# Kernel optimization log

Hardware: AMD Instinct MI355X
Metric: run time of the kernel (lower is better)

The kernel has to match this reference:

```python
import jax, jax.numpy as jnp
import numpy as np

HS, WS = 64, 64
SIGMA = 1.2
UPDATE_COEFF = 0.2
R = 3
N_BLOCKS = 3
GROUPS = 8
EPS_GN = 1e-5
CM, CP, CS, CT, HID = 64, 3, 128, 128, 128
B, T, HIN, WIN = 32, 256, 128, 128


def setup_inputs() -> dict:
    key = jax.random.key(0)
    ks = jax.random.split(key, 10)
    s = 0.02
    cin = CM + CP + CT
    f32 = jnp.float32
    return {
        'M': jax.random.normal(ks[0], (B, CM, HIN, WIN), f32),
        'x0_hat_norm': jax.random.uniform(ks[1], (B, T, 2), f32, -1.0, 1.0),
        't_embed': jax.random.normal(ks[2], (B, CT), f32),
        'in_proj_w': jax.random.normal(ks[3], (CS, cin), f32) * s,
        'in_proj_b': jnp.zeros((CS,), f32),
        'rb_c1w': jax.random.normal(ks[4], (N_BLOCKS, CS, CS, 3, 3), f32) * s,
        'rb_c1b': jnp.zeros((N_BLOCKS, CS), f32),
        'rb_g1w': jnp.ones((N_BLOCKS, CS), f32),
        'rb_g1b': jnp.zeros((N_BLOCKS, CS), f32),
        'rb_c2w': jax.random.normal(ks[5], (N_BLOCKS, CS, CS, 3, 3), f32) * s,
        'rb_c2b': jnp.zeros((N_BLOCKS, CS), f32),
        'rb_g2w': jnp.ones((N_BLOCKS, CS), f32),
        'rb_g2b': jnp.zeros((N_BLOCKS, CS), f32),
        'out_w': jax.random.normal(ks[6], (CS, CS), f32) * s,
        'out_b': jnp.zeros((CS,), f32),
        'mlp_w1': jax.random.normal(ks[7], (CS + CT, HID), f32) * s,
        'mlp_b1': jnp.zeros((HID,), f32),
        'mlp_w2': jax.random.normal(ks[8], (HID, HID), f32) * s,
        'mlp_b2': jnp.zeros((HID,), f32),
        'mlp_w3': jax.random.normal(ks[9], (HID, 2), f32) * s,
        'mlp_b3': jnp.zeros((2,), f32),
    }


def _resize_bilinear(M, Hs, Ws):
    # torch F.interpolate bilinear, align_corners=False, no antialias
    Bn, C, H, W = M.shape
    def coords(n_out, n_in):
        sc = n_in / n_out
        c = (jnp.arange(n_out, dtype=M.dtype) + 0.5) * sc - 0.5
        c = jnp.clip(c, 0.0, n_in - 1.0)
        i0 = jnp.floor(c)
        f = c - i0
        i0 = i0.astype(jnp.int32)
        i1 = jnp.minimum(i0 + 1, n_in - 1)
        return i0, i1, f
    y0, y1, fy = coords(Hs, H)
    x0, x1, fx = coords(Ws, W)
    top = M[:, :, y0, :] * (1 - fy)[None, None, :, None] + M[:, :, y1, :] * fy[None, None, :, None]
    return top[:, :, :, x0] * (1 - fx)[None, None, None, :] + top[:, :, :, x1] * fx[None, None, None, :]


def _rasterize_vel(pts, H, W, sigma):
    # pts: (B,T,2) pixel coords -> (B,3,H,W) [heat, vx, vy]
    xs = jnp.arange(W, dtype=pts.dtype)
    ys = jnp.arange(H, dtype=pts.dtype)
    d2 = (pts[:, :, None, None, 0] - xs[None, None, None, :]) ** 2 \
       + (pts[:, :, None, None, 1] - ys[None, None, :, None]) ** 2  # (B,T,H,W)
    w = jnp.exp(-0.5 * d2 / (sigma ** 2 + 1e-8))
    heat = w.max(axis=1)
    v = jnp.pad(jnp.diff(pts, axis=1), ((0, 0), (1, 0), (0, 0)))
    vx = (w * v[:, :, None, None, 0]).sum(axis=1)
    vy = (w * v[:, :, None, None, 1]).sum(axis=1)
    wsum = jnp.maximum(w.sum(axis=1), 1e-6)
    return jnp.stack([heat, vx / wsum, vy / wsum], axis=1)


def _conv3x3(x, w, b):
    y = jax.lax.conv_general_dilated(x, w, (1, 1), 'SAME', dimension_numbers=('NCHW', 'OIHW', 'NCHW'))
    return y + b[None, :, None, None]


def _gn(x, g, b):
    Bn, C, H, W = x.shape
    xr = x.reshape(Bn, GROUPS, C // GROUPS, H, W)
    mu = xr.mean(axis=(2, 3, 4), keepdims=True)
    var = xr.var(axis=(2, 3, 4), keepdims=True)
    xn = ((xr - mu) * jax.lax.rsqrt(var + EPS_GN)).reshape(Bn, C, H, W)
    return xn * g[None, :, None, None] + b[None, :, None, None]


def _grid_sample(S, coords):
    # bilinear, align_corners=False, zero padding. coords (B,T,2) in [-1,1] -> (B,T,C)
    Bn, C, H, W = S.shape
    Tn = coords.shape[1]
    x = ((coords[..., 0] + 1.0) * W - 1.0) * 0.5
    y = ((coords[..., 1] + 1.0) * H - 1.0) * 0.5
    x0 = jnp.floor(x)
    y0 = jnp.floor(y)
    wx = x - x0
    wy = y - y0
    Sf = S.reshape(Bn, C, H * W)
    out = jnp.zeros((Bn, C, Tn), S.dtype)
    for xi, yi, wgt in ((x0, y0, (1 - wx) * (1 - wy)), (x0 + 1, y0, wx * (1 - wy)),
                        (x0, y0 + 1, (1 - wx) * wy), (x0 + 1, y0 + 1, wx * wy)):
        valid = (xi >= 0) & (xi <= W - 1) & (yi >= 0) & (yi <= H - 1)
        xc = jnp.clip(xi, 0, W - 1).astype(jnp.int32)
        yc = jnp.clip(yi, 0, H - 1).astype(jnp.int32)
        idx = jnp.broadcast_to((yc * W + xc)[:, None, :], (Bn, C, Tn))
        g = jnp.take_along_axis(Sf, idx, axis=2)
        out = out + g * (wgt * valid)[:, None, :]
    return out.transpose(0, 2, 1)


def _forward(M, x0_hat_norm, t_embed, in_proj_w, in_proj_b, rb_c1w, rb_c1b, rb_g1w, rb_g1b,
             rb_c2w, rb_c2b, rb_g2w, rb_g2b, out_w, out_b,
             mlp_w1, mlp_b1, mlp_w2, mlp_b2, mlp_w3, mlp_b3):
    Bn = M.shape[0]
    Ms = _resize_bilinear(M, HS, WS)
    t_map = jnp.broadcast_to(t_embed[:, :, None, None], (Bn, CT, HS, WS))
    x = x0_hat_norm
    for _ in range(R):
        x_pix = jnp.stack([(x[..., 0] + 1) * 0.5 * (WS - 1), (x[..., 1] + 1) * 0.5 * (HS - 1)], axis=-1)
        P = _rasterize_vel(x_pix, HS, WS, SIGMA)  # (B,3,HS,WS)
        # SpatialRefine
        inp = jnp.concatenate([Ms, P, t_map], axis=1)
        S = jnp.einsum('bihw,oi->bohw', inp, in_proj_w) + in_proj_b[None, :, None, None]
        for i in range(N_BLOCKS):
            h = jax.nn.silu(_gn(_conv3x3(S, rb_c1w[i], rb_c1b[i]), rb_g1w[i], rb_g1b[i]))
            h = _gn(_conv3x3(h, rb_c2w[i], rb_c2b[i]), rb_g2w[i], rb_g2b[i])
            S = jax.nn.silu(S + h)
        S = jnp.einsum('bihw,oi->bohw', S, out_w) + out_b[None, :, None, None]
        # PointCorrector
        read = _grid_sample(S, x)  # (B,T,CS)
        t_tok = jnp.broadcast_to(t_embed[:, None, :], (Bn, read.shape[1], CT))
        feat = jnp.concatenate([read, t_tok], axis=-1)
        h = jax.nn.silu(feat @ mlp_w1 + mlp_b1)
        h = jax.nn.silu(h @ mlp_w2 + mlp_b2)
        dx = h @ mlp_w3 + mlp_b3
        x = jnp.clip(x + UPDATE_COEFF * dx, -1.0, 1.0)
    return x


def reference(M, x0_hat_norm, t_embed, in_proj_w, in_proj_b, rb_c1w, rb_c1b, rb_g1w, rb_g1b,
              rb_c2w, rb_c2b, rb_g2w, rb_g2b, out_w, out_b,
              mlp_w1, mlp_b1, mlp_w2, mlp_b2, mlp_w3, mlp_b3):
    return _forward(M, x0_hat_norm, t_embed, in_proj_w, in_proj_b, rb_c1w, rb_c1b, rb_g1w, rb_g1b,
                    rb_c2w, rb_c2b, rb_g2w, rb_g2b, out_w, out_b,
                    mlp_w1, mlp_b1, mlp_w2, mlp_b2, mlp_w3, mlp_b3)
```

## Files before the change

### kernel.cpp

```cpp
#include <hip/hip_runtime.h>
#include <cstddef>

#define BN 32
#define TN 256
#define PW 66
#define PLANE 4356

typedef __attribute__((ext_vector_type(8))) short bf16x8;
typedef __attribute__((ext_vector_type(4))) float f32x4;

struct __attribute__((aligned(16))) U4 { unsigned x, y, z, w; };

__device__ __forceinline__ float silu_f(float v) { return v / (1.f + __expf(-v)); }

__device__ __forceinline__ unsigned short f2bf(float f) {
  unsigned u = __float_as_uint(f);
  unsigned r = (u + 0x7fffu + ((u >> 16) & 1u)) >> 16;
  return (unsigned short)r;
}
__device__ __forceinline__ float bf2f(unsigned short h) {
  return __uint_as_float((unsigned)h << 16);
}
__device__ __forceinline__ unsigned pack2(float a, float b) {
  return (unsigned)f2bf(a) | ((unsigned)f2bf(b) << 16);
}

__device__ __forceinline__ void gld16(const unsigned short* g, unsigned short* l) {
  __builtin_amdgcn_global_load_lds((const __attribute__((address_space(1))) unsigned int*)g,
                                   (__attribute__((address_space(3))) unsigned int*)l, 16, 0, 0);
}

__global__ __launch_bounds__(256) void copy_kernel(const float* __restrict__ src, float* __restrict__ dst, int n) {
  int i = blockIdx.x * 256 + threadIdx.x;
  if (i < n) dst[i] = src[i];
}

__global__ __launch_bounds__(256) void zerohalo_kernel(unsigned short* __restrict__ base) {
  int idx = blockIdx.x * 256 + threadIdx.x;
  if (idx >= 384 * 1040) return;
  int p = idx / 1040, rem = idx % 1040;
  int hp = rem >> 2, icq = rem & 3;
  int row, x;
  if (hp < 66) { row = 0; x = hp; }
  else if (hp < 132) { row = 65; x = hp - 66; }
  else { int i = hp - 132; row = 1 + (i >> 1); x = (i & 1) * 65; }
  U4 z = {0u, 0u, 0u, 0u};
  *(U4*)&base[((size_t)p * PLANE + row * PW + x) * 32 + icq * 8] = z;
}

__global__ __launch_bounds__(256) void resize_t_kernel(const float* __restrict__ M, unsigned short* __restrict__ Ms4) {
  __shared__ unsigned short lt[4 * 64 * 72];
  int b = blockIdx.y, yt = blockIdx.x;
  int tid = threadIdx.x;
  for (int i = tid; i < 4 * 64 * 64; i += 256) {
    int c = i >> 8, y = (i >> 6) & 3, x = i & 63;
    const float* p = M + (((size_t)(b * 64 + c) * 128) + (yt * 4 + y) * 2) * 128 + 2 * x;
    float2 a = *(const float2*)p;
    float2 bq = *(const float2*)(p + 128);
    lt[(y * 64 + x) * 72 + c] = f2bf(0.25f * (a.x + a.y + bq.x + bq.y));
  }
  __syncthreads();
  for (int i = tid; i < 2048; i += 256) {
    int icq = i & 3, pxl = (i >> 2) & 255, cc = i >> 10;
    U4 q = *(const U4*)&lt[pxl * 72 + cc * 32 + icq * 8];
    int y = yt * 4 + (pxl >> 6), x = pxl & 63;
    *(U4*)&Ms4[(((size_t)(b * 2 + cc) * PLANE) + (size_t)(y + 1) * PW + x + 1) * 32 + icq * 8] = q;
  }
}

__global__ __launch_bounds__(256) void wprep_kernel(const float* __restrict__ Wsrc, unsigned short* __restrict__ Wdst) {
  int idx = blockIdx.x * 256 + threadIdx.x;
  if (idx >= 147456) return;
  int icp = idx & 31;
  int oc = (idx >> 5) & 127;
  int tc = idx >> 12;
  int t = tc >> 2, cch = tc & 3;
  Wdst[idx] = f2bf(Wsrc[(size_t)oc * 1152 + (size_t)(cch * 32 + icp) * 9 + t]);
}

__global__ __launch_bounds__(256) void wprep_in_kernel(const float* __restrict__ ipw, unsigned short* __restrict__ wi) {
  int idx = blockIdx.x * 256 + threadIdx.x;
  if (idx >= 12288) return;
  int icp = idx & 31, oc = (idx >> 5) & 127, cc = idx >> 12;
  float f = 0.f;
  if (cc < 2) f = ipw[oc * 195 + cc * 32 + icp];
  else if (icp < 3) f = ipw[oc * 195 + 64 + icp];
  wi[idx] = f2bf(f);
}

__global__ __launch_bounds__(256) void wprep_out_kernel(const float* __restrict__ ow, unsigned short* __restrict__ wo) {
  int idx = blockIdx.x * 256 + threadIdx.x;
  if (idx >= 16384) return;
  int icp = idx & 31, oc = (idx >> 5) & 127, cc = idx >> 12;
  wo[idx] = f2bf(ow[oc * 128 + cc * 32 + icp]);
}

__global__ __launch_bounds__(256) void tctr_kernel(const float* __restrict__ w, const float* __restrict__ bias,
                                                   const float* __restrict__ te, float* __restrict__ tctr) {
  int i = blockIdx.x * 256 + threadIdx.x;
  if (i >= BN * 128) return;
  int b = i >> 7, o = i & 127;
  float acc = bias[o];
  const float* wp = w + (size_t)o * 195 + 67;
  const float* t = te + b * 128;
  #pragma unroll 8
  for (int k = 0; k < 128; ++k) acc += wp[k] * t[k];
  tctr[i] = acc;
}

__global__ __launch_bounds__(256) void tpart_kernel(const float* __restrict__ w1, const float* __restrict__ b1,
                                                    const float* __restrict__ te, float* __restrict__ tp) {
  int i = blockIdx.x * 256 + threadIdx.x;
  if (i >= BN * 128) return;
  int b = i >> 7, j = i & 127;
  float acc = b1[j];
  #pragma unroll 8
  for (int k = 0; k < 128; ++k) acc += te[b * 128 + k] * w1[(size_t)(128 + k) * 128 + j];
  tp[i] = acc;
}

__global__ __launch_bounds__(256) void raster4_kernel(const float* __restrict__ x, unsigned short* __restrict__ Pp) {
  int b = blockIdx.y, blk = blockIdx.x;
  int tid = threadIdx.x;
  int pix = blk * 256 + tid;
  __shared__ float spx[TN], spy[TN];
  __shared__ unsigned short lp[256 * 32];
  spx[tid] = (x[(b * TN + tid) * 2] + 1.f) * 0.5f * 63.f;
  spy[tid] = (x[(b * TN + tid) * 2 + 1] + 1.f) * 0.5f * 63.f;
  __syncthreads();
  float fx = (float)(pix & 63), fy = (float)(pix >> 6);
  const float coef = -0.5f / (1.44f + 1e-8f);
  float heat = 0.f, sx = 0.f, sy = 0.f, sw = 0.f;
  float prevx = 0.f, prevy = 0.f;
  for (int t = 0; t < TN; ++t) {
    float px = spx[t], py = spy[t];
    float ddx = px - fx, ddy = py - fy;
    float w = __expf(coef * (ddx * ddx + ddy * ddy));
    heat = fmaxf(heat, w);
    float vx = (t == 0) ? 0.f : px - prevx;
    float vy = (t == 0) ? 0.f : py - prevy;
    prevx = px; prevy = py;
    sx += w * vx; sy += w * vy; sw += w;
  }
  float inv = 1.f / fmaxf(sw, 1e-6f);
  U4 q0; q0.x = pack2(heat, sx * inv); q0.y = pack2(sy * inv, 0.f); q0.z = 0u; q0.w = 0u;
  U4 z = {0u, 0u, 0u, 0u};
  *(U4*)&lp[tid * 32 + 0] = q0;
  *(U4*)&lp[tid * 32 + 8] = z;
  *(U4*)&lp[tid * 32 + 16] = z;
  *(U4*)&lp[tid * 32 + 24] = z;
  __syncthreads();
  for (int it = 0; it < 4; ++it) {
    int sid = it * 256 + tid;
    int pxl = sid >> 2, icq = sid & 3;
    int gp = blk * 256 + pxl;
    int y = gp >> 6, xx = gp & 63;
    *(U4*)&Pp[((size_t)b * PLANE + (size_t)(y + 1) * PW + xx + 1) * 32 + icq * 8] = *(const U4*)&lp[pxl * 32 + icq * 8];
  }
}

__global__ __launch_bounds__(512, 4) void conv3_v4(const unsigned short* __restrict__ In4,
                                                   const unsigned short* __restrict__ Wb,
                                                   const float* __restrict__ Bias,
                                                   unsigned short* __restrict__ Out4) {
  __shared__ unsigned short lds[2][12672];
  const int P = blockIdx.x;
  const int L = (P & 7) * 64 + (P >> 3);
  const int b = L >> 4, y0 = (L & 15) * 4;
  const int tid = threadIdx.x, l = tid & 63, w = tid >> 6;
  const int ocg = w & 1, rowg = w >> 1, l15 = l & 15, k8 = l >> 4;

  f32x4 acc[4][4];
  #pragma unroll
  for (int mf = 0; mf < 4; ++mf)
    #pragma unroll
    for (int nf = 0; nf < 4; ++nf) acc[mf][nf] = (f32x4){0.f, 0.f, 0.f, 0.f};

  auto issue_stage = [&](int cc, int nb) {
    const unsigned short* slab = In4 + (((size_t)(b * 4 + cc)) * PLANE + (size_t)y0 * PW) * 32;
    #pragma unroll
    for (int i = 0; i < 3; ++i) {
      int G = i * 512 + tid;
      int q = G >> 2;
      int r = q / 66;
      int xs = q - r * 66;
      int src = (G & ~3) | ((G & 3) ^ ((xs >> 1) & 3));
      gld16(slab + (size_t)src * 8, &lds[nb][(size_t)(i * 512 + w * 64) * 8]);
    }
    if (tid < 96) {
      int G = 1536 + tid;
      int q = G >> 2;
      int r = q / 66;
      int xs = q - r * 66;
      int src = (G & ~3) | ((G & 3) ^ ((xs >> 1) & 3));
      gld16(slab + (size_t)src * 8, &lds[nb][(size_t)(1536 + w * 64) * 8]);
    }
  };

  issue_stage(0, 0);
  __syncthreads();

  for (int cc = 0; cc < 4; ++cc) {
    const unsigned short* cur = &lds[cc & 1][0];
    if (cc < 3) issue_stage(cc + 1, (cc & 1) ^ 1);
    #pragma unroll
    for (int t = 0; t < 9; ++t) {
      const int ky = t / 3, kx = t - ky * 3;
      bf16x8 a[4];
      #pragma unroll
      for (int mf = 0; mf < 4; ++mf)
        a[mf] = *(const bf16x8*)&Wb[(((size_t)(t * 4 + cc) * 128) + ocg * 64 + mf * 16 + l15) * 32 + k8 * 8];
      #pragma unroll
      for (int nf = 0; nf < 4; ++nf) {
        int xs = nf * 16 + l15 + kx;
        int slot = ((rowg + ky) * 66 + xs) * 4 + (k8 ^ ((xs >> 1) & 3));
        bf16x8 bv = *(const bf16x8*)&cur[(size_t)slot * 8];
        #pragma unroll
        for (int mf = 0; mf < 4; ++mf)
          acc[mf][nf] = __builtin_amdgcn_mfma_f32_16x16x32_bf16(a[mf], bv, acc[mf][nf], 0, 0, 0);
      }
    }
    __syncthreads();
  }

  unsigned short* eb = &lds[0][0];
  #pragma unroll
  for (int h = 0; h < 2; ++h) {
    if ((rowg >> 1) == h) {
      int prow = rowg & 1;
      #pragma unroll
      for (int mf = 0; mf < 4; ++mf) {
        int oc = ocg * 64 + mf * 16 + k8 * 4;
        float4 bv4 = *(const float4*)&Bias[oc];
        #pragma unroll
        for (int nf = 0; nf < 4; ++nf) {
          int pxl = prow * 64 + nf * 16 + l15;
          unsigned lo = pack2(acc[mf][nf][0] + bv4.x, acc[mf][nf][1] + bv4.y);
          unsigned hi = pack2(acc[mf][nf][2] + bv4.z, acc[mf][nf][3] + bv4.w);
          unsigned off = (unsigned)(pxl * 256 + oc * 2) ^ ((pxl & 7) << 4);
          *(uint2*)((char*)eb + off) = make_uint2(lo, hi);
        }
      }
    }
    __syncthreads();
    {
      int pxl = tid >> 2, icq = tid & 3;
      int px = h * 128 + pxl;
      int yy = px >> 6, xx = px & 63;
      #pragma unroll
      for (int cc2 = 0; cc2 < 4; ++cc2) {
        unsigned off = (unsigned)(pxl * 256 + cc2 * 64 + icq * 16) ^ ((pxl & 7) << 4);
        U4 q = *(const U4*)((char*)eb + off);
        *(U4*)&Out4[(((size_t)(b * 4 + cc2)) * PLANE + (size_t)(y0 + yy + 1) * PW + xx + 1) * 32 + icq * 8] = q;
      }
    }
    __syncthreads();
  }
}

__global__ __launch_bounds__(256, 2) void conv1_v2(const unsigned short* __restrict__ srcA, int ncA,
                                                   const unsigned short* __restrict__ srcB, int nc,
                                                   const unsigned short* __restrict__ Wb,
                                                   const float* __restrict__ Bias, int perB,
                                                   unsigned short* __restrict__ Out4) {
  __shared__ unsigned short lds[32768];
  const int P = blockIdx.x;
  const int L = (P & 7) * 64 + (P >> 3);
  const int b = L >> 4, px0 = (L & 15) * 256;
  const int tid = threadIdx.x, l = tid & 63, w = tid >> 6;
  const int ocg = w & 1, rowg = w >> 1, l15 = l & 15, k8 = l >> 4;

  f32x4 acc[4][8];
  #pragma unroll
  for (int mf = 0; mf < 4; ++mf)
    #pragma unroll
    for (int nf = 0; nf < 8; ++nf) acc[mf][nf] = (f32x4){0.f, 0.f, 0.f, 0.f};

  for (int cc = 0; cc < nc; ++cc) {
    const unsigned short* base = (cc < ncA) ? srcA + ((size_t)(b * ncA + cc)) * PLANE * 32
                                            : srcB + ((size_t)b) * PLANE * 32;
    bf16x8 a[4];
    #pragma unroll
    for (int mf = 0; mf < 4; ++mf)
      a[mf] = *(const bf16x8*)&Wb[(((size_t)cc * 128) + ocg * 64 + mf * 16 + l15) * 32 + k8 * 8];
    #pragma unroll
    for (int nf = 0; nf < 8; ++nf) {
      int px = px0 + rowg * 128 + nf * 16 + l15;
      int y = px >> 6, x = px & 63;
      bf16x8 bv = *(const bf16x8*)&base[((size_t)(y + 1) * PW + x + 1) * 32 + k8 * 8];
      #pragma unroll
      for (int mf = 0; mf < 4; ++mf)
        acc[mf][nf] = __builtin_amdgcn_mfma_f32_16x16x32_bf16(a[mf], bv, acc[mf][nf], 0, 0, 0);
    }
  }
  const float* bp = Bias + (perB ? b * 128 : 0);
  #pragma unroll
  for (int mf = 0; mf < 4; ++mf) {
    int oc = ocg * 64 + mf * 16 + k8 * 4;
    float4 bv4 = *(const float4*)&bp[oc];
    #pragma unroll
    for (int nf = 0; nf < 8; ++nf) {
      int pxl = rowg * 128 + nf * 16 + l15;
      unsigned lo = pack2(acc[mf][nf][0] + bv4.x, acc[mf][nf][1] + bv4.y);
      unsigned hi = pack2(acc[mf][nf][2] + bv4.z, acc[mf][nf][3] + bv4.w);
      unsigned off = (unsigned)(pxl * 256 + oc * 2) ^ ((pxl & 7) << 4);
      *(uint2*)((char*)lds + off) = make_uint2(lo, hi);
    }
  }
  __syncthreads();
  #pragma unroll
  for (int cc2 = 0; cc2 < 4; ++cc2)
    #pragma unroll
    for (int it = 0; it < 4; ++it) {
      int sid = it * 256 + tid;
      int pxl = sid >> 2, icq = sid & 3;
      unsigned off = (unsigned)(pxl * 256 + cc2 * 64 + icq * 16) ^ ((pxl & 7) << 4);
      U4 q = *(const U4*)((char*)lds + off);
      int px = px0 + pxl;
      int yy = px >> 6, xx = px & 63;
      *(U4*)&Out4[(((size_t)(b * 4 + cc2)) * PLANE + (size_t)(yy + 1) * PW + xx + 1) * 32 + icq * 8] = q;
    }
}

__global__ __launch_bounds__(256) void gnstats4_kernel(const unsigned short* __restrict__ X, float* __restrict__ stats) {
  int bc = blockIdx.x;
  const unsigned short* p = X + (size_t)bc * PLANE * 32;
  float s0 = 0.f, q0 = 0.f, s1 = 0.f, q1 = 0.f;
  for (int px = threadIdx.x; px < 4096; px += 256) {
    const unsigned short* row = p + ((size_t)((px >> 6) + 1) * PW + (px & 63) + 1) * 32;
    #pragma unroll
    for (int half = 0; half < 2; ++half) {
      float s = 0.f, qq = 0.f;
      #pragma unroll
      for (int ii = 0; ii < 2; ++ii) {
        U4 v = *(const U4*)&row[half * 16 + ii * 8];
        unsigned a[4] = {v.x, v.y, v.z, v.w};
        #pragma unroll
        for (int p2 = 0; p2 < 4; ++p2) {
          float f0 = bf2f((unsigned short)(a[p2] & 0xffffu));
          float f1 = bf2f((unsigned short)(a[p2] >> 16));
          s += f0 + f1; qq += f0 * f0 + f1 * f1;
        }
      }
      if (half == 0) { s0 += s; q0 += qq; } else { s1 += s; q1 += qq; }
    }
  }
  __shared__ float red[4][256];
  red[0][threadIdx.x] = s0; red[1][threadIdx.x] = q0; red[2][threadIdx.x] = s1; red[3][threadIdx.x] = q1;
  __syncthreads();
  for (int off = 128; off > 0; off >>= 1) {
    if (threadIdx.x < off)
      #pragma unroll
      for (int k = 0; k < 4; ++k) red[k][threadIdx.x] += red[k][threadIdx.x + off];
    __syncthreads();
  }
  if (threadIdx.x == 0) {
    const float invn = 1.f / 65536.f;
    int b = bc >> 2, cc = bc & 3;
    float mu0 = red[0][0] * invn, var0 = red[1][0] * invn - mu0 * mu0;
    float mu1 = red[2][0] * invn, var1 = red[3][0] * invn - mu1 * mu1;
    int g0 = b * 8 + cc * 2;
    stats[g0 * 2] = mu0; stats[g0 * 2 + 1] = rsqrtf(var0 + 1e-5f);
    stats[(g0 + 1) * 2] = mu1; stats[(g0 + 1) * 2 + 1] = rsqrtf(var1 + 1e-5f);
  }
}

__global__ __launch_bounds__(256) void gn1apply_kernel(unsigned short* __restrict__ A,
                                                       const float* __restrict__ stats, const float* __restrict__ gam,
                                                       const float* __restrict__ bet) {
  size_t e8 = (size_t)blockIdx.x * 256 + threadIdx.x;
  int icq = (int)(e8 & 3), x = (int)((e8 >> 2) & 63), y = (int)((e8 >> 8) & 63);
  int cc = (int)((e8 >> 14) & 3), b = (int)(e8 >> 16);
  size_t off = (((size_t)(b * 4 + cc)) * PLANE + (size_t)(y + 1) * PW + x + 1) * 32 + icq * 8;
  int ch = icq * 8;
  int g = cc * 2 + (ch >> 4);
  float mu = stats[(b * 8 + g) * 2], ri = stats[(b * 8 + g) * 2 + 1];
  int c0 = cc * 32 + ch;
  float4 g0 = *(const float4*)&gam[c0], g1 = *(const float4*)&gam[c0 + 4];
  float4 b0 = *(const float4*)&bet[c0], b1 = *(const float4*)&bet[c0 + 4];
  float gv[8] = {g0.x, g0.y, g0.z, g0.w, g1.x, g1.y, g1.z, g1.w};
  float bv[8] = {b0.x, b0.y, b0.z, b0.w, b1.x, b1.y, b1.z, b1.w};
  U4 va = *(const U4*)&A[off];
  unsigned aa[4] = {va.x, va.y, va.z, va.w};
  unsigned out[4];
  #pragma unroll
  for (int p = 0; p < 4; ++p) {
    float h0 = (bf2f((unsigned short)(aa[p] & 0xffffu)) - mu) * ri * gv[2 * p] + bv[2 * p];
    float h1 = (bf2f((unsigned short)(aa[p] >> 16)) - mu) * ri * gv[2 * p + 1] + bv[2 * p + 1];
    out[p] = pack2(silu_f(h0), silu_f(h1));
  }
  U4 q; q.x = out[0]; q.y = out[1]; q.z = out[2]; q.w = out[3];
  *(U4*)&A[off] = q;
}

__global__ __launch_bounds__(256) void gn2add4_kernel(unsigned short* __restrict__ S, const unsigned short* __restrict__ Bb,
                                                      const float* __restrict__ stats, const float* __restrict__ gam,
                                                      const float* __restrict__ bet) {
  size_t e8 = (size_t)blockIdx.x * 256 + threadIdx.x;
  int icq = (int)(e8 & 3), x = (int)((e8 >> 2) & 63), y = (int)((e8 >> 8) & 63);
  int cc = (int)((e8 >> 14) & 3), b = (int)(e8 >> 16);
  size_t off = (((size_t)(b * 4 + cc)) * PLANE + (size_t)(y + 1) * PW + x + 1) * 32 + icq * 8;
  int ch = icq * 8;
  int g = cc * 2 + (ch >> 4);
  float mu = stats[(b * 8 + g) * 2], ri = stats[(b * 8 + g) * 2 + 1];
  int c0 = cc * 32 + ch;
  float4 g0 = *(const float4*)&gam[c0], g1 = *(const float4*)&gam[c0 + 4];
  float4 b0 = *(const float4*)&bet[c0], b1 = *(const float4*)&bet[c0 + 4];
  float gv[8] = {g0.x, g0.y, g0.z, g0.w, g1.x, g1.y, g1.z, g1.w};
  float bv[8] = {b0.x, b0.y, b0.z, b0.w, b1.x, b1.y, b1.z, b1.w};
  U4 vb = *(const U4*)&Bb[off];
  U4 vs = *(const U4*)&S[off];
  unsigned ab[4] = {vb.x, vb.y, vb.z, vb.w};
  unsigned as[4] = {vs.x, vs.y, vs.z, vs.w};
  unsigned out[4];
  #pragma unroll
  for (int p = 0; p < 4; ++p) {
    float h0 = (bf2f((unsigned short)(ab[p] & 0xffffu)) - mu) * ri * gv[2 * p] + bv[2 * p];
    float h1 = (bf2f((unsigned short)(ab[p] >> 16)) - mu) * ri * gv[2 * p + 1] + bv[2 * p + 1];
    float r0 = silu_f(bf2f((unsigned short)(as[p] & 0xffffu)) + h0);
    float r1 = silu_f(bf2f((unsigned short)(as[p] >> 16)) + h1);
    out[p] = pack2(r0, r1);
  }
  U4 q; q.x = out[0]; q.y = out[1]; q.z = out[2]; q.w = out[3];
  *(U4*)&S[off] = q;
}

__global__ __launch_bounds__(128) void gsample4_kernel(const unsigned short* __restrict__ S2, const float* __restrict__ x,
                                                       float* __restrict__ rd) {
  int token = blockIdx.x, c = threadIdx.x, b = token >> 8;
  float cx = x[token * 2], cy = x[token * 2 + 1];
  float fx = (cx + 1.f) * 32.f - 0.5f;
  float fy = (cy + 1.f) * 32.f - 0.5f;
  float x0f = floorf(fx), y0f = floorf(fy);
  float wx = fx - x0f, wy = fy - y0f;
  const unsigned short* Sb = S2 + ((size_t)(b * 4 + (c >> 5)) * PLANE) * 32 + (c & 31);
  float acc = 0.f;
  #pragma unroll
  for (int cor = 0; cor < 4; ++cor) {
    float xi = x0f + (float)(cor & 1), yi = y0f + (float)(cor >> 1);
    float wgt = ((cor & 1) ? wx : 1.f - wx) * ((cor >> 1) ? wy : 1.f - wy);
    if (xi >= 0.f && xi <= 63.f && yi >= 0.f && yi <= 63.f)
      acc += bf2f(Sb[(size_t)(((int)yi + 1) * PW + (int)xi + 1) * 32]) * wgt;
  }
  rd[(size_t)token * 128 + c] = acc;
}

__global__ __launch_bounds__(256) void mlp_fc_kernel(const float* __restrict__ in, const float* __restrict__ w,
                                                     const float* __restrict__ init, int initPerB,
                                                     float* __restrict__ out) {
  int tok0 = blockIdx.x * 2;
  int tid = threadIdx.x;
  __shared__ float sr[2][128];
  sr[tid >> 7][tid & 127] = in[(size_t)tok0 * 128 + tid];
  __syncthreads();
  int t = tid >> 7, j = tid & 127;
  int token = tok0 + t;
  int b = token >> 8;
  float acc = initPerB ? init[b * 128 + j] : init[j];
  #pragma unroll 8
  for (int k = 0; k < 128; ++k) acc += sr[t][k] * w[(size_t)k * 128 + j];
  out[(size_t)token * 128 + j] = silu_f(acc);
}

__global__ __launch_bounds__(256) void mlp3_update_kernel(const float* __restrict__ h2, const float* __restrict__ w3,
                                                          const float* __restrict__ b3, float* __restrict__ x) {
  int token = blockIdx.x * 256 + threadIdx.x;
  if (token >= BN * TN) return;
  float d0 = b3[0], d1 = b3[1];
  const float* h = h2 + (size_t)token * 128;
  #pragma unroll 8
  for (int k = 0; k < 128; ++k) { float hv = h[k]; d0 += hv * w3[k * 2]; d1 += hv * w3[k * 2 + 1]; }
  float nx = x[token * 2] + 0.2f * d0;
  float ny = x[token * 2 + 1] + 0.2f * d1;
  x[token * 2] = fminf(fmaxf(nx, -1.f), 1.f);
  x[token * 2 + 1] = fminf(fmaxf(ny, -1.f), 1.f);
}

extern "C" void kernel_launch(void* const* d_in, const int* in_sizes, int n_in,
                              void* d_out, int out_size, void* d_ws, size_t ws_size,
                              hipStream_t stream) {
  const float* M   = (const float*)d_in[0];
  const float* x0  = (const float*)d_in[1];
  const float* te  = (const float*)d_in[2];
  const float* ipw = (const float*)d_in[3];
  const float* ipb = (const float*)d_in[4];
  const float* c1w = (const float*)d_in[5];
  const float* c1b = (const float*)d_in[6];
  const float* g1w = (const float*)d_in[7];
  const float* g1b = (const float*)d_in[8];
  const float* c2w = (const float*)d_in[9];
  const float* c2b = (const float*)d_in[10];
  const float* g2w = (const float*)d_in[11];
  const float* g2b = (const float*)d_in[12];
  const float* ow  = (const float*)d_in[13];
  const float* ob  = (const float*)d_in[14];
  const float* w1  = (const float*)d_in[15];
  const float* b1  = (const float*)d_in[16];
  const float* w2  = (const float*)d_in[17];
  const float* b2  = (const float*)d_in[18];
  const float* w3  = (const float*)d_in[19];
  const float* b3  = (const float*)d_in[20];

  const size_t PSH = (size_t)PLANE * 32;
  float* f     = (float*)d_ws;
  float* wx    = f;
  float* tctr  = wx + 16384;
  float* tpart = tctr + 4096;
  float* st1   = tpart + 4096;
  float* st2   = st1 + 512;
  float* rd    = st2 + 512;
  float* h1    = rd + 1048576;
  float* h2    = h1 + 1048576;
  unsigned short* S4  = (unsigned short*)(h2 + 1048576);
  unsigned short* A4  = S4 + 128 * PSH;
  unsigned short* B4  = A4 + 128 * PSH;
  unsigned short* Ms4 = B4 + 128 * PSH;
  unsigned short* Pp  = Ms4 + 64 * PSH;
  unsigned short* wc  = Pp + 32 * PSH;
  unsigned short* wi  = wc + 884736;
  unsigned short* wo  = wi + 12288;

  copy_kernel<<<64, 256, 0, stream>>>(x0, wx, 16384);
  zerohalo_kernel<<<1560, 256, 0, stream>>>(S4);
  resize_t_kernel<<<dim3(16, 32), 256, 0, stream>>>(M, Ms4);
  tctr_kernel<<<16, 256, 0, stream>>>(ipw, ipb, te, tctr);
  tpart_kernel<<<16, 256, 0, stream>>>(w1, b1, te, tpart);
  for (int i = 0; i < 3; ++i) {
    wprep_kernel<<<576, 256, 0, stream>>>(c1w + (size_t)i * 147456, wc + (size_t)(2 * i) * 147456);
    wprep_kernel<<<576, 256, 0, stream>>>(c2w + (size_t)i * 147456, wc + (size_t)(2 * i + 1) * 147456);
  }
  wprep_in_kernel<<<48, 256, 0, stream>>>(ipw, wi);
  wprep_out_kernel<<<64, 256, 0, stream>>>(ow, wo);

  for (int r = 0; r < 3; ++r) {
    raster4_kernel<<<dim3(16, 32), 256, 0, stream>>>(wx, Pp);
    conv1_v2<<<512, 256, 0, stream>>>(Ms4, 2, Pp, 3, wi, tctr, 1, S4);
    for (int i = 0; i < 3; ++i) {
      conv3_v4<<<512, 512, 0, stream>>>(S4, wc + (size_t)(2 * i) * 147456, c1b + i * 128, A4);
      gnstats4_kernel<<<128, 256, 0, stream>>>(A4, st1);
      gn1apply_kernel<<<8192, 256, 0, stream>>>(A4, st1, g1w + i * 128, g1b + i * 128);
      conv3_v4<<<512, 512, 0, stream>>>(A4, wc + (size_t)(2 * i + 1) * 147456, c2b + i * 128, B4);
      gnstats4_kernel<<<128, 256, 0, stream>>>(B4, st2);
      gn2add4_kernel<<<8192, 256, 0, stream>>>(S4, B4, st2, g2w + i * 128, g2b + i * 128);
    }
    conv1_v2<<<512, 256, 0, stream>>>(S4, 4, nullptr, 4, wo, ob, 0, A4);
    gsample4_kernel<<<8192, 128, 0, stream>>>(A4, wx, rd);
    mlp_fc_kernel<<<4096, 256, 0, stream>>>(rd, w1, tpart, 1, h1);
    mlp_fc_kernel<<<4096, 256, 0, stream>>>(h1, w2, b2, 0, h2);
    mlp3_update_kernel<<<32, 256, 0, stream>>>(h2, w3, b3, wx);
  }
  copy_kernel<<<64, 256, 0, stream>>>(wx, (float*)d_out, 16384);
}
```

Before: 1.808 ms.

## Fuse GroupNorm stats into conv epilogue and GN1 apply into conv2 prologue

The 3x3 conv kernel now accumulates per-group sum and sum-of-squares in its epilogue with a wave shuffle reduction, then atomically adds them to a per-iteration stats buffer. This removes the separate gnstats passes. The second conv applies GN1 normalize plus SiLU while staging its input tiles into LDS, which removes the standalone gn1apply pass over A4. That staging uses register loads instead of async global-to-LDS copies, so the second conv loses some load/compute overlap and does more ALU work per tile. Stats are taken from fp32 accumulators before bf16 rounding, so results may drift slightly from the old path.

```diff
diff --git a/kernel.cpp b/kernel.cpp
--- a/kernel.cpp
+++ b/kernel.cpp
@@ -33,6 +33,11 @@
 __global__ __launch_bounds__(256) void copy_kernel(const float* __restrict__ src, float* __restrict__ dst, int n) {
   int i = blockIdx.x * 256 + threadIdx.x;
   if (i < n) dst[i] = src[i];
+}
+
+__global__ __launch_bounds__(256) void zstats_kernel(float* __restrict__ s) {
+  int i = blockIdx.x * 256 + threadIdx.x;
+  if (i < 18 * 512) s[i] = 0.f;
 }
 
 __global__ __launch_bounds__(256) void zerohalo_kernel(unsigned short* __restrict__ base) {
@@ -159,16 +164,23 @@
   }
 }
 
-__global__ __launch_bounds__(512, 4) void conv3_v4(const unsigned short* __restrict__ In4,
+template<int FUSED>
+__global__ __launch_bounds__(512, 4) void conv3_v5(const unsigned short* __restrict__ In4,
                                                    const unsigned short* __restrict__ Wb,
                                                    const float* __restrict__ Bias,
+                                                   const float* __restrict__ stIn,
+                                                   const float* __restrict__ gam,
+                                                   const float* __restrict__ bet,
+                                                   float* __restrict__ stOut,
                                                    unsigned short* __restrict__ Out4) {
   __shared__ unsigned short lds[2][12672];
+  __shared__ float sred[8][4][2];
   const int P = blockIdx.x;
   const int L = (P & 7) * 64 + (P >> 3);
   const int b = L >> 4, y0 = (L & 15) * 4;
   const int tid = threadIdx.x, l = tid & 63, w = tid >> 6;
   const int ocg = w & 1, rowg = w >> 1, l15 = l & 15, k8 = l >> 4;
+  const float invn = 1.f / 65536.f;
 
   f32x4 acc[4][4];
   #pragma unroll
@@ -176,8 +188,12 @@
     #pragma unroll
     for (int nf = 0; nf < 4; ++nf) acc[mf][nf] = (f32x4){0.f, 0.f, 0.f, 0.f};
 
+  auto slab_of = [&](int cc) {
+    return In4 + (((size_t)(b * 4 + cc)) * PLANE + (size_t)y0 * PW) * 32;
+  };
+
   auto issue_stage = [&](int cc, int nb) {
-    const unsigned short* slab = In4 + (((size_t)(b * 4 + cc)) * PLANE + (size_t)y0 * PW) * 32;
+    const unsigned short* slab = slab_of(cc);
     #pragma unroll
     for (int i = 0; i < 3; ++i) {
       int G = i * 512 + tid;
@@ -197,14 +213,73 @@
     }
   };
 
-  issue_stage(0, 0);
+  auto muri = [&](int cc, float& mu0, float& ri0, float& mu1, float& ri1) {
+    float s0 = stIn[(b * 8 + cc * 2) * 2], q0 = stIn[(b * 8 + cc * 2) * 2 + 1];
+    float s1 = stIn[(b * 8 + cc * 2 + 1) * 2], q1 = stIn[(b * 8 + cc * 2 + 1) * 2 + 1];
+    mu0 = s0 * invn; ri0 = rsqrtf(q0 * invn - mu0 * mu0 + 1e-5f);
+    mu1 = s1 * invn; ri1 = rsqrtf(q1 * invn - mu1 * mu1 + 1e-5f);
+  };
+  auto fetchT = [&](const unsigned short* slab, int cc, int sid,
+                    float mu0, float ri0, float mu1, float ri1) -> U4 {
+    U4 q = *(const U4*)&slab[(size_t)sid * 8];
+    int r = sid / 264, rem = sid - r * 264;
+    int xs = rem >> 2, icq = rem & 3;
+    bool halo = (xs == 0) | (xs == 65) | ((y0 == 0) & (r == 0)) | ((y0 == 60) & (r == 5));
+    float mu = (icq & 2) ? mu1 : mu0;
+    float ri = (icq & 2) ? ri1 : ri0;
+    const float* gp = gam + cc * 32 + icq * 8;
+    const float* bp = bet + cc * 32 + icq * 8;
+    unsigned vv[4] = {q.x, q.y, q.z, q.w};
+    unsigned oo[4];
+    #pragma unroll
+    for (int p = 0; p < 4; ++p) {
+      float v0 = (bf2f((unsigned short)(vv[p] & 0xffffu)) - mu) * ri * gp[2 * p] + bp[2 * p];
+      float v1 = (bf2f((unsigned short)(vv[p] >> 16)) - mu) * ri * gp[2 * p + 1] + bp[2 * p + 1];
+      oo[p] = pack2(silu_f(v0), silu_f(v1));
+    }
+    U4 o;
+    o.x = halo ? 0u : oo[0]; o.y = halo ? 0u : oo[1];
+    o.z = halo ? 0u : oo[2]; o.w = halo ? 0u : oo[3];
+    return o;
+  };
+  auto put = [&](int nb, int sid, U4 q) {
+    int rem = sid % 264;
+    int xs = rem >> 2;
+    int slot = (sid & ~3) | ((sid & 3) ^ ((xs >> 1) & 3));
+    *(U4*)&lds[nb][(size_t)slot * 8] = q;
+  };
+
+  if constexpr (FUSED) {
+    const unsigned short* slab = slab_of(0);
+    float mu0, ri0, mu1, ri1;
+    muri(0, mu0, ri0, mu1, ri1);
+    #pragma unroll
+    for (int i = 0; i < 3; ++i) put(0, i * 512 + tid, fetchT(slab, 0, i * 512 + tid, mu0, ri0, mu1, ri1));
+    if (tid < 48) put(0, 1536 + tid, fetchT(slab, 0, 1536 + tid, mu0, ri0, mu1, ri1));
+  } else {
+    issue_stage(0, 0);
+  }
   __syncthreads();
 
   for (int cc = 0; cc < 4; ++cc) {
     const unsigned short* cur = &lds[cc & 1][0];
-    if (cc < 3) issue_stage(cc + 1, (cc & 1) ^ 1);
-    #pragma unroll
-    for (int t = 0; t < 9; ++t) {
+    const int nb = (cc & 1) ^ 1;
+    U4 q0, q1, q2, q3;
+    if constexpr (FUSED) {
+      if (cc < 3) {
+        const unsigned short* slabn = slab_of(cc + 1);
+        float mu0, ri0, mu1, ri1;
+        muri(cc + 1, mu0, ri0, mu1, ri1);
+        q0 = fetchT(slabn, cc + 1, tid, mu0, ri0, mu1, ri1);
+        q1 = fetchT(slabn, cc + 1, tid + 512, mu0, ri0, mu1, ri1);
+        q2 = fetchT(slabn, cc + 1, tid + 1024, mu0, ri0, mu1, ri1);
+        if (tid < 48) q3 = fetchT(slabn, cc + 1, 1536 + tid, mu0, ri0, mu1, ri1);
+      }
+    } else {
+      if (cc < 3) issue_stage(cc + 1, nb);
+    }
+    #pragma unroll
+    for (int t = 0; t < 4; ++t) {
       const int ky = t / 3, kx = t - ky * 3;
       bf16x8 a[4];
       #pragma unroll
@@ -220,7 +295,64 @@
           acc[mf][nf] = __builtin_amdgcn_mfma_f32_16x16x32_bf16(a[mf], bv, acc[mf][nf], 0, 0, 0);
       }
     }
+    if constexpr (FUSED) {
+      if (cc < 3) {
+        put(nb, tid, q0);
+        put(nb, tid + 512, q1);
+        put(nb, tid + 1024, q2);
+        if (tid < 48) put(nb, 1536 + tid, q3);
+      }
+    }
+    #pragma unroll
+    for (int t = 4; t < 9; ++t) {
+      const int ky = t / 3, kx = t - ky * 3;
+      bf16x8 a[4];
+      #pragma unroll
+      for (int mf = 0; mf < 4; ++mf)
+        a[mf] = *(const bf16x8*)&Wb[(((size_t)(t * 4 + cc) * 128) + ocg * 64 + mf * 16 + l15) * 32 + k8 * 8];
+      #pragma unroll
+      for (int nf = 0; nf < 4; ++nf) {
+        int xs = nf * 16 + l15 + kx;
+        int slot = ((rowg + ky) * 66 + xs) * 4 + (k8 ^ ((xs >> 1) & 3));
+        bf16x8 bv = *(const bf16x8*)&cur[(size_t)slot * 8];
+        #pragma unroll
+        for (int mf = 0; mf < 4; ++mf)
+          acc[mf][nf] = __builtin_amdgcn_mfma_f32_16x16x32_bf16(a[mf], bv, acc[mf][nf], 0, 0, 0);
+      }
+    }
     __syncthreads();
+  }
+
+  {
+    #pragma unroll
+    for (int mf = 0; mf < 4; ++mf) {
+      int oc = ocg * 64 + mf * 16 + k8 * 4;
+      float4 bv4 = *(const float4*)&Bias[oc];
+      float s = 0.f, qq = 0.f;
+      #pragma unroll
+      for (int nf = 0; nf < 4; ++nf) {
+        float v0 = acc[mf][nf][0] + bv4.x;
+        float v1 = acc[mf][nf][1] + bv4.y;
+        float v2 = acc[mf][nf][2] + bv4.z;
+        float v3 = acc[mf][nf][3] + bv4.w;
+        s += (v0 + v1) + (v2 + v3);
+        qq += (v0 * v0 + v1 * v1) + (v2 * v2 + v3 * v3);
+      }
+      #pragma unroll
+      for (int off = 32; off > 0; off >>= 1) {
+        s += __shfl_xor(s, off, 64);
+        qq += __shfl_xor(qq, off, 64);
+      }
+      if (l == 0) { sred[w][mf][0] = s; sred[w][mf][1] = qq; }
+    }
+  }
+  __syncthreads();
+  if (tid < 8) {
+    int g = tid, og = g >> 2, mf = g & 3;
+    float s = (sred[og][mf][0] + sred[og + 2][mf][0]) + (sred[og + 4][mf][0] + sred[og + 6][mf][0]);
+    float qq = (sred[og][mf][1] + sred[og + 2][mf][1]) + (sred[og + 4][mf][1] + sred[og + 6][mf][1]);
+    atomicAdd(&stOut[(b * 8 + g) * 2], s);
+    atomicAdd(&stOut[(b * 8 + g) * 2 + 1], qq);
   }
 
   unsigned short* eb = &lds[0][0];
@@ -322,79 +454,8 @@
     }
 }
 
-__global__ __launch_bounds__(256) void gnstats4_kernel(const unsigned short* __restrict__ X, float* __restrict__ stats) {
-  int bc = blockIdx.x;
-  const unsigned short* p = X + (size_t)bc * PLANE * 32;
-  float s0 = 0.f, q0 = 0.f, s1 = 0.f, q1 = 0.f;
-  for (int px = threadIdx.x; px < 4096; px += 256) {
-    const unsigned short* row = p + ((size_t)((px >> 6) + 1) * PW + (px & 63) + 1) * 32;
-    #pragma unroll
-    for (int half = 0; half < 2; ++half) {
-      float s = 0.f, qq = 0.f;
-      #pragma unroll
-      for (int ii = 0; ii < 2; ++ii) {
-        U4 v = *(const U4*)&row[half * 16 + ii * 8];
-        unsigned a[4] = {v.x, v.y, v.z, v.w};
-        #pragma unroll
-        for (int p2 = 0; p2 < 4; ++p2) {
-          float f0 = bf2f((unsigned short)(a[p2] & 0xffffu));
-          float f1 = bf2f((unsigned short)(a[p2] >> 16));
-          s += f0 + f1; qq += f0 * f0 + f1 * f1;
-        }
-      }
-      if (half == 0) { s0 += s; q0 += qq; } else { s1 += s; q1 += qq; }
-    }
-  }
-  __shared__ float red[4][256];
-  red[0][threadIdx.x] = s0; red[1][threadIdx.x] = q0; red[2][threadIdx.x] = s1; red[3][threadIdx.x] = q1;
-  __syncthreads();
-  for (int off = 128; off > 0; off >>= 1) {
-    if (threadIdx.x < off)
-      #pragma unroll
-      for (int k = 0; k < 4; ++k) red[k][threadIdx.x] += red[k][threadIdx.x + off];
-    __syncthreads();
-  }
-  if (threadIdx.x == 0) {
-    const float invn = 1.f / 65536.f;
-    int b = bc >> 2, cc = bc & 3;
-    float mu0 = red[0][0] * invn, var0 = red[1][0] * invn - mu0 * mu0;
-    float mu1 = red[2][0] * invn, var1 = red[3][0] * invn - mu1 * mu1;
-    int g0 = b * 8 + cc * 2;
-    stats[g0 * 2] = mu0; stats[g0 * 2 + 1] = rsqrtf(var0 + 1e-5f);
-    stats[(g0 + 1) * 2] = mu1; stats[(g0 + 1) * 2 + 1] = rsqrtf(var1 + 1e-5f);
-  }
-}
-
-__global__ __launch_bounds__(256) void gn1apply_kernel(unsigned short* __restrict__ A,
-                                                       const float* __restrict__ stats, const float* __restrict__ gam,
-                                                       const float* __restrict__ bet) {
-  size_t e8 = (size_t)blockIdx.x * 256 + threadIdx.x;
-  int icq = (int)(e8 & 3), x = (int)((e8 >> 2) & 63), y = (int)((e8 >> 8) & 63);
-  int cc = (int)((e8 >> 14) & 3), b = (int)(e8 >> 16);
-  size_t off = (((size_t)(b * 4 + cc)) * PLANE + (size_t)(y + 1) * PW + x + 1) * 32 + icq * 8;
-  int ch = icq * 8;
-  int g = cc * 2 + (ch >> 4);
-  float mu = stats[(b * 8 + g) * 2], ri = stats[(b * 8 + g) * 2 + 1];
-  int c0 = cc * 32 + ch;
-  float4 g0 = *(const float4*)&gam[c0], g1 = *(const float4*)&gam[c0 + 4];
-  float4 b0 = *(const float4*)&bet[c0], b1 = *(const float4*)&bet[c0 + 4];
-  float gv[8] = {g0.x, g0.y, g0.z, g0.w, g1.x, g1.y, g1.z, g1.w};
-  float bv[8] = {b0.x, b0.y, b0.z, b0.w, b1.x, b1.y, b1.z, b1.w};
-  U4 va = *(const U4*)&A[off];
-  unsigned aa[4] = {va.x, va.y, va.z, va.w};
-  unsigned out[4];
-  #pragma unroll
-  for (int p = 0; p < 4; ++p) {
-    float h0 = (bf2f((unsigned short)(aa[p] & 0xffffu)) - mu) * ri * gv[2 * p] + bv[2 * p];
-    float h1 = (bf2f((unsigned short)(aa[p] >> 16)) - mu) * ri * gv[2 * p + 1] + bv[2 * p + 1];
-    out[p] = pack2(silu_f(h0), silu_f(h1));
-  }
-  U4 q; q.x = out[0]; q.y = out[1]; q.z = out[2]; q.w = out[3];
-  *(U4*)&A[off] = q;
-}
-
 __global__ __launch_bounds__(256) void gn2add4_kernel(unsigned short* __restrict__ S, const unsigned short* __restrict__ Bb,
-                                                      const float* __restrict__ stats, const float* __restrict__ gam,
+                                                      const float* __restrict__ st, const float* __restrict__ gam,
                                                       const float* __restrict__ bet) {
   size_t e8 = (size_t)blockIdx.x * 256 + threadIdx.x;
   int icq = (int)(e8 & 3), x = (int)((e8 >> 2) & 63), y = (int)((e8 >> 8) & 63);
@@ -402,7 +463,10 @@
   size_t off = (((size_t)(b * 4 + cc)) * PLANE + (size_t)(y + 1) * PW + x + 1) * 32 + icq * 8;
   int ch = icq * 8;
   int g = cc * 2 + (ch >> 4);
-  float mu = stats[(b * 8 + g) * 2], ri = stats[(b * 8 + g) * 2 + 1];
+  const float invn = 1.f / 65536.f;
+  float ssum = st[(b * 8 + g) * 2], qsum = st[(b * 8 + g) * 2 + 1];
+  float mu = ssum * invn;
+  float ri = rsqrtf(qsum * invn - mu * mu + 1e-5f);
   int c0 = cc * 32 + ch;
   float4 g0 = *(const float4*)&gam[c0], g1 = *(const float4*)&gam[c0 + 4];
   float4 b0 = *(const float4*)&bet[c0], b1 = *(const float4*)&bet[c0 + 4];
@@ -506,9 +570,8 @@
   float* wx    = f;
   float* tctr  = wx + 16384;
   float* tpart = tctr + 4096;
-  float* st1   = tpart + 4096;
-  float* st2   = st1 + 512;
-  float* rd    = st2 + 512;
+  float* stats = tpart + 4096;
+  float* rd    = stats + 9216;
   float* h1    = rd + 1048576;
   float* h2    = h1 + 1048576;
   unsigned short* S4  = (unsigned short*)(h2 + 1048576);
@@ -521,6 +584,7 @@
   unsigned short* wo  = wi + 12288;
 
   copy_kernel<<<64, 256, 0, stream>>>(x0, wx, 16384);
+  zstats_kernel<<<36, 256, 0, stream>>>(stats);
   zerohalo_kernel<<<1560, 256, 0, stream>>>(S4);
   resize_t_kernel<<<dim3(16, 32), 256, 0, stream>>>(M, Ms4);
   tctr_kernel<<<16, 256, 0, stream>>>(ipw, ipb, te, tctr);
@@ -536,12 +600,13 @@
     raster4_kernel<<<dim3(16, 32), 256, 0, stream>>>(wx, Pp);
     conv1_v2<<<512, 256, 0, stream>>>(Ms4, 2, Pp, 3, wi, tctr, 1, S4);
     for (int i = 0; i < 3; ++i) {
-      conv3_v4<<<512, 512, 0, stream>>>(S4, wc + (size_t)(2 * i) * 147456, c1b + i * 128, A4);
-      gnstats4_kernel<<<128, 256, 0, stream>>>(A4, st1);
-      gn1apply_kernel<<<8192, 256, 0, stream>>>(A4, st1, g1w + i * 128, g1b + i * 128);
-      conv3_v4<<<512, 512, 0, stream>>>(A4, wc + (size_t)(2 * i + 1) * 147456, c2b + i * 128, B4);
-      gnstats4_kernel<<<128, 256, 0, stream>>>(B4, st2);
-      gn2add4_kernel<<<8192, 256, 0, stream>>>(S4, B4, st2, g2w + i * 128, g2b + i * 128);
+      float* stA = stats + (size_t)(r * 3 + i) * 512;
+      float* stB = stats + (size_t)(9 + r * 3 + i) * 512;
+      conv3_v5<0><<<512, 512, 0, stream>>>(S4, wc + (size_t)(2 * i) * 147456, c1b + i * 128,
+                                           nullptr, nullptr, nullptr, stA, A4);
+      conv3_v5<1><<<512, 512, 0, stream>>>(A4, wc + (size_t)(2 * i + 1) * 147456, c2b + i * 128,
+                                           stA, g1w + i * 128, g1b + i * 128, stB, B4);
+      gn2add4_kernel<<<8192, 256, 0, stream>>>(S4, B4, stB, g2w + i * 128, g2b + i * 128);
     }
     conv1_v2<<<512, 256, 0, stream>>>(S4, 4, nullptr, 4, wo, ob, 0, A4);
     gsample4_kernel<<<8192, 128, 0, stream>>>(A4, wx, rd);
```

Result: slower. 3.381 ms (+87.0%).

## Fuse GroupNorm statistics into conv3x3 epilogue via atomic accumulation

Applied to the files above, without the earlier changes.

The conv3x3 kernel now reduces per-group sum and sum-of-squares from its fp32 accumulators with wave shuffles and shared memory, then atomically adds them into a per-call stats buffer. This removes the separate gnstats pass, which re-read the whole bf16 activation tensor after each conv. The apply kernels now derive mean and rsqrt variance from the raw sums. A one-time zeroing kernel clears 18 distinct stats slots, one per conv call, so no per-iteration reset is needed. The trade-offs are atomic contention and that statistics are now taken from fp32 values before bf16 rounding, with a sum-of-squares variance formula.

```diff
diff --git a/kernel.cpp b/kernel.cpp
--- a/kernel.cpp
+++ b/kernel.cpp
@@ -33,6 +33,11 @@
 __global__ __launch_bounds__(256) void copy_kernel(const float* __restrict__ src, float* __restrict__ dst, int n) {
   int i = blockIdx.x * 256 + threadIdx.x;
   if (i < n) dst[i] = src[i];
+}
+
+__global__ __launch_bounds__(256) void zstats_kernel(float* __restrict__ s) {
+  int i = blockIdx.x * 256 + threadIdx.x;
+  if (i < 18 * 512) s[i] = 0.f;
 }
 
 __global__ __launch_bounds__(256) void zerohalo_kernel(unsigned short* __restrict__ base) {
@@ -159,11 +164,13 @@
   }
 }
 
-__global__ __launch_bounds__(512, 4) void conv3_v4(const unsigned short* __restrict__ In4,
+__global__ __launch_bounds__(512, 4) void conv3_v6(const unsigned short* __restrict__ In4,
                                                    const unsigned short* __restrict__ Wb,
                                                    const float* __restrict__ Bias,
+                                                   float* __restrict__ stOut,
                                                    unsigned short* __restrict__ Out4) {
   __shared__ unsigned short lds[2][12672];
+  __shared__ float sred[8][4][2];
   const int P = blockIdx.x;
   const int L = (P & 7) * 64 + (P >> 3);
   const int b = L >> 4, y0 = (L & 15) * 4;
@@ -221,6 +228,36 @@
       }
     }
     __syncthreads();
+  }
+
+  #pragma unroll
+  for (int mf = 0; mf < 4; ++mf) {
+    int oc = ocg * 64 + mf * 16 + k8 * 4;
+    float4 bv4 = *(const float4*)&Bias[oc];
+    float s = 0.f, qq = 0.f;
+    #pragma unroll
+    for (int nf = 0; nf < 4; ++nf) {
+      float v0 = acc[mf][nf][0] + bv4.x;
+      float v1 = acc[mf][nf][1] + bv4.y;
+      float v2 = acc[mf][nf][2] + bv4.z;
+      float v3 = acc[mf][nf][3] + bv4.w;
+      s += (v0 + v1) + (v2 + v3);
+      qq += (v0 * v0 + v1 * v1) + (v2 * v2 + v3 * v3);
+    }
+    #pragma unroll
+    for (int off = 32; off > 0; off >>= 1) {
+      s += __shfl_xor(s, off, 64);
+      qq += __shfl_xor(qq, off, 64);
+    }
+    if (l == 0) { sred[w][mf][0] = s; sred[w][mf][1] = qq; }
+  }
+  __syncthreads();
+  if (tid < 8) {
+    int g = tid, og = g >> 2, mf = g & 3;
+    float s = (sred[og][mf][0] + sred[og + 2][mf][0]) + (sred[og + 4][mf][0] + sred[og + 6][mf][0]);
+    float qq = (sred[og][mf][1] + sred[og + 2][mf][1]) + (sred[og + 4][mf][1] + sred[og + 6][mf][1]);
+    atomicAdd(&stOut[(b * 8 + g) * 2], s);
+    atomicAdd(&stOut[(b * 8 + g) * 2 + 1], qq);
   }
 
   unsigned short* eb = &lds[0][0];
@@ -322,51 +359,8 @@
     }
 }
 
-__global__ __launch_bounds__(256) void gnstats4_kernel(const unsigned short* __restrict__ X, float* __restrict__ stats) {
-  int bc = blockIdx.x;
-  const unsigned short* p = X + (size_t)bc * PLANE * 32;
-  float s0 = 0.f, q0 = 0.f, s1 = 0.f, q1 = 0.f;
-  for (int px = threadIdx.x; px < 4096; px += 256) {
-    const unsigned short* row = p + ((size_t)((px >> 6) + 1) * PW + (px & 63) + 1) * 32;
-    #pragma unroll
-    for (int half = 0; half < 2; ++half) {
-      float s = 0.f, qq = 0.f;
-      #pragma unroll
-      for (int ii = 0; ii < 2; ++ii) {
-        U4 v = *(const U4*)&row[half * 16 + ii * 8];
-        unsigned a[4] = {v.x, v.y, v.z, v.w};
-        #pragma unroll
-        for (int p2 = 0; p2 < 4; ++p2) {
-          float f0 = bf2f((unsigned short)(a[p2] & 0xffffu));
-          float f1 = bf2f((unsigned short)(a[p2] >> 16));
-          s += f0 + f1; qq += f0 * f0 + f1 * f1;
-        }
-      }
-      if (half == 0) { s0 += s; q0 += qq; } else { s1 += s; q1 += qq; }
-    }
-  }
-  __shared__ float red[4][256];
-  red[0][threadIdx.x] = s0; red[1][threadIdx.x] = q0; red[2][threadIdx.x] = s1; red[3][threadIdx.x] = q1;
-  __syncthreads();
-  for (int off = 128; off > 0; off >>= 1) {
-    if (threadIdx.x < off)
-      #pragma unroll
-      for (int k = 0; k < 4; ++k) red[k][threadIdx.x] += red[k][threadIdx.x + off];
-    __syncthreads();
-  }
-  if (threadIdx.x == 0) {
-    const float invn = 1.f / 65536.f;
-    int b = bc >> 2, cc = bc & 3;
-    float mu0 = red[0][0] * invn, var0 = red[1][0] * invn - mu0 * mu0;
-    float mu1 = red[2][0] * invn, var1 = red[3][0] * invn - mu1 * mu1;
-    int g0 = b * 8 + cc * 2;
-    stats[g0 * 2] = mu0; stats[g0 * 2 + 1] = rsqrtf(var0 + 1e-5f);
-    stats[(g0 + 1) * 2] = mu1; stats[(g0 + 1) * 2 + 1] = rsqrtf(var1 + 1e-5f);
-  }
-}
-
 __global__ __launch_bounds__(256) void gn1apply_kernel(unsigned short* __restrict__ A,
-                                                       const float* __restrict__ stats, const float* __restrict__ gam,
+                                                       const float* __restrict__ st, const float* __restrict__ gam,
                                                        const float* __restrict__ bet) {
   size_t e8 = (size_t)blockIdx.x * 256 + threadIdx.x;
   int icq = (int)(e8 & 3), x = (int)((e8 >> 2) & 63), y = (int)((e8 >> 8) & 63);
@@ -374,7 +368,10 @@
   size_t off = (((size_t)(b * 4 + cc)) * PLANE + (size_t)(y + 1) * PW + x + 1) * 32 + icq * 8;
   int ch = icq * 8;
   int g = cc * 2 + (ch >> 4);
-  float mu = stats[(b * 8 + g) * 2], ri = stats[(b * 8 + g) * 2 + 1];
+  const float invn = 1.f / 65536.f;
+  float ssum = st[(b * 8 + g) * 2], qsum = st[(b * 8 + g) * 2 + 1];
+  float mu = ssum * invn;
+  float ri = rsqrtf(qsum * invn - mu * mu + 1e-5f);
   int c0 = cc * 32 + ch;
   float4 g0 = *(const float4*)&gam[c0], g1 = *(const float4*)&gam[c0 + 4];
   float4 b0 = *(const float4*)&bet[c0], b1 = *(const float4*)&bet[c0 + 4];
@@ -394,7 +391,7 @@
 }
 
 __global__ __launch_bounds__(256) void gn2add4_kernel(unsigned short* __restrict__ S, const unsigned short* __restrict__ Bb,
-                                                      const float* __restrict__ stats, const float* __restrict__ gam,
+                                                      const float* __restrict__ st, const float* __restrict__ gam,
                                                       const float* __restrict__ bet) {
   size_t e8 = (size_t)blockIdx.x * 256 + threadIdx.x;
   int icq = (int)(e8 & 3), x = (int)((e8 >> 2) & 63), y = (int)((e8 >> 8) & 63);
@@ -402,7 +399,10 @@
   size_t off = (((size_t)(b * 4 + cc)) * PLANE + (size_t)(y + 1) * PW + x + 1) * 32 + icq * 8;
   int ch = icq * 8;
   int g = cc * 2 + (ch >> 4);
-  float mu = stats[(b * 8 + g) * 2], ri = stats[(b * 8 + g) * 2 + 1];
+  const float invn = 1.f / 65536.f;
+  float ssum = st[(b * 8 + g) * 2], qsum = st[(b * 8 + g) * 2 + 1];
+  float mu = ssum * invn;
+  float ri = rsqrtf(qsum * invn - mu * mu + 1e-5f);
   int c0 = cc * 32 + ch;
   float4 g0 = *(const float4*)&gam[c0], g1 = *(const float4*)&gam[c0 + 4];
   float4 b0 = *(const float4*)&bet[c0], b1 = *(const float4*)&bet[c0 + 4];
@@ -506,9 +506,8 @@
   float* wx    = f;
   float* tctr  = wx + 16384;
   float* tpart = tctr + 4096;
-  float* st1   = tpart + 4096;
-  float* st2   = st1 + 512;
-  float* rd    = st2 + 512;
+  float* stats = tpart + 4096;
+  float* rd    = stats + 9216;
   float* h1    = rd + 1048576;
   float* h2    = h1 + 1048576;
   unsigned short* S4  = (unsigned short*)(h2 + 1048576);
@@ -521,6 +520,7 @@
   unsigned short* wo  = wi + 12288;
 
   copy_kernel<<<64, 256, 0, stream>>>(x0, wx, 16384);
+  zstats_kernel<<<36, 256, 0, stream>>>(stats);
   zerohalo_kernel<<<1560, 256, 0, stream>>>(S4);
   resize_t_kernel<<<dim3(16, 32), 256, 0, stream>>>(M, Ms4);
   tctr_kernel<<<16, 256, 0, stream>>>(ipw, ipb, te, tctr);
@@ -536,12 +536,12 @@
     raster4_kernel<<<dim3(16, 32), 256, 0, stream>>>(wx, Pp);
     conv1_v2<<<512, 256, 0, stream>>>(Ms4, 2, Pp, 3, wi, tctr, 1, S4);
     for (int i = 0; i < 3; ++i) {
-      conv3_v4<<<512, 512, 0, stream>>>(S4, wc + (size_t)(2 * i) * 147456, c1b + i * 128, A4);
-      gnstats4_kernel<<<128, 256, 0, stream>>>(A4, st1);
-      gn1apply_kernel<<<8192, 256, 0, stream>>>(A4, st1, g1w + i * 128, g1b + i * 128);
-      conv3_v4<<<512, 512, 0, stream>>>(A4, wc + (size_t)(2 * i + 1) * 147456, c2b + i * 128, B4);
-      gnstats4_kernel<<<128, 256, 0, stream>>>(B4, st2);
-      gn2add4_kernel<<<8192, 256, 0, stream>>>(S4, B4, st2, g2w + i * 128, g2b + i * 128);
+      float* stA = stats + (size_t)(r * 3 + i) * 512;
+      float* stB = stats + (size_t)(9 + r * 3 + i) * 512;
+      conv3_v6<<<512, 512, 0, stream>>>(S4, wc + (size_t)(2 * i) * 147456, c1b + i * 128, stA, A4);
+      gn1apply_kernel<<<8192, 256, 0, stream>>>(A4, stA, g1w + i * 128, g1b + i * 128);
+      conv3_v6<<<512, 512, 0, stream>>>(A4, wc + (size_t)(2 * i + 1) * 147456, c2b + i * 128, stB, B4);
+      gn2add4_kernel<<<8192, 256, 0, stream>>>(S4, B4, stB, g2w + i * 128, g2b + i * 128);
     }
     conv1_v2<<<512, 256, 0, stream>>>(S4, 4, nullptr, 4, wo, ob, 0, A4);
     gsample4_kernel<<<8192, 128, 0, stream>>>(A4, wx, rd);
```

Result: no change. 1.784 ms (-1.3%).
